# Performance work log

Hardware: AMD Instinct MI355X
Metric: run time of the kernel (lower is better)

Reference implementation:

```python
import jax, jax.numpy as jnp
import numpy as np
import math

B, L, D, H = 2, 2048, 1024, 16
DT = D // H  # d_tensor per head


def setup_inputs() -> dict:
    key = jax.random.key(0)
    ks = jax.random.split(key, 14)
    s = 1.0 / math.sqrt(D)
    return {
        "Q": jax.random.normal(ks[0], (B, L, D), jnp.float32),
        "K": jax.random.normal(ks[1], (B, L, D), jnp.float32),
        "V": jax.random.normal(ks[2], (B, L, D), jnp.float32),
        "mask": jax.random.randint(ks[3], (B, L, L), 0, 2, jnp.int32),
        "attn_bias": jax.random.normal(ks[4], (1, H, L, L), jnp.float32),
        "Wq": jax.random.normal(ks[5], (D, D), jnp.float32) * s,
        "bq": jnp.zeros((D,), jnp.float32),
        "Wk": jax.random.normal(ks[6], (D, D), jnp.float32) * s,
        "bk": jnp.zeros((D,), jnp.float32),
        "Wv": jax.random.normal(ks[7], (D, D), jnp.float32) * s,
        "bv": jnp.zeros((D,), jnp.float32),
        "Wo": jax.random.normal(ks[8], (D, D), jnp.float32) * s,
        "bo": jnp.zeros((D,), jnp.float32),
    }


def _split(x):
    # (B, L, D) -> (B, H, L, DT)
    b, l, d = x.shape
    return x.reshape(b, l, H, DT).transpose(0, 2, 1, 3)


def reference(Q, K, V, mask, attn_bias, Wq, bq, Wk, bk, Wv, bv, Wo, bo):
    # Linear projections (torch nn.Linear: x @ W.T + b)
    q = _split(Q @ Wq.T + bq)  # (B, H, L, DT)
    k = _split(K @ Wk.T + bk)
    v = _split(V @ Wv.T + bv)
    scale = 1.0 / math.sqrt(DT)
    score = jnp.einsum("bhqd,bhkd->bhqk", q, k) * scale  # (B, H, L, L)
    # masked_fill(mask==0, -10000), mask broadcast over heads
    score = jnp.where(mask[:, None, :, :] == 0, jnp.float32(-10000.0), score)
    # encoder path: additive attn_bias (is_dec_layer=False)
    score = score + attn_bias
    p = jax.nn.softmax(score, axis=-1)
    out = jnp.einsum("bhqk,bhkd->bhqd", p, v)  # (B, H, L, DT)
    out = out.transpose(0, 2, 1, 3).reshape(Q.shape[0], Q.shape[1], D)
    return out @ Wo.T + bo
```

## Files before the change

kernel.cpp:

```cpp
#include <hip/hip_runtime.h>
#include <hip/hip_bf16.h>

#define NB 2
#define NL 2048
#define ND 1024
#define NH 16
#define NDT 64
#define SZE ((size_t)NB * NL * ND)
#define WSZE ((size_t)ND * ND)

typedef unsigned short u16;
typedef unsigned int u32;
typedef unsigned long long u64;

typedef __attribute__((ext_vector_type(8))) short s16x8;
typedef __attribute__((ext_vector_type(4))) float f32x4;
typedef __attribute__((ext_vector_type(4))) u16 u16x4;
typedef __attribute__((ext_vector_type(8))) u16 u16x8;

static __device__ __forceinline__ u16 f2b(float f) {
  union { float f; u32 u; } x; x.f = f;
  u32 r = x.u + 0x7fffu + ((x.u >> 16) & 1u);
  return (u16)(r >> 16);
}

static __device__ __forceinline__ int swz(int r, int cb) {
  return r * 128 + (cb ^ ((r & 7) << 4));
}

static __device__ __forceinline__ void gl16(const void* g, void* l) {
  __builtin_amdgcn_global_load_lds(
      (const __attribute__((address_space(1))) unsigned int*)g,
      (__attribute__((address_space(3))) unsigned int*)l, 16, 0, 0);
}

static __device__ __forceinline__ u16x8 pack8(f32x4 a, f32x4 b) {
  u16x8 r;
  r[0] = f2b(a[0]); r[1] = f2b(a[1]); r[2] = f2b(a[2]); r[3] = f2b(a[3]);
  r[4] = f2b(b[0]); r[5] = f2b(b[1]); r[6] = f2b(b[2]); r[7] = f2b(b[3]);
  return r;
}

static __device__ __forceinline__ u64 ldg_v2(const u64* p) {
  u64 r;
  asm volatile("global_load_dwordx2 %0, %1, off" : "=v"(r) : "v"(p) : "memory");
  return r;
}

__global__ __launch_bounds__(256)
void conv_k(const float* __restrict__ q, const float* __restrict__ k,
            const float* __restrict__ v, const float* __restrict__ wq,
            const float* __restrict__ wk, const float* __restrict__ wv,
            const float* __restrict__ wo, u16* __restrict__ cin,
            u16* __restrict__ cw)
{
  const int z = blockIdx.z;
  const float* s; u16* d; size_t n;
  if (z < 3) { s = (z == 0) ? q : (z == 1) ? k : v; d = cin + (size_t)z * SZE; n = SZE; }
  else { int m = z - 3; s = (m == 0) ? wq : (m == 1) ? wk : (m == 2) ? wv : wo; d = cw + (size_t)m * WSZE; n = WSZE; }
  size_t i = ((size_t)blockIdx.x * 256 + threadIdx.x) * 8;
  if (i >= n) return;
  f32x4 a = *reinterpret_cast<const f32x4*>(s + i);
  f32x4 b = *reinterpret_cast<const f32x4*>(s + i + 4);
  *reinterpret_cast<u16x8*>(d + i) = pack8(a, b);
}

__global__ __launch_bounds__(256)
void maskpack_k(const int* __restrict__ mask, u64* __restrict__ mb) {
  const int lane = threadIdx.x & 63;
  const int gw = (blockIdx.x * 256 + threadIdx.x) >> 6;
  const int nw = (gridDim.x * 256) >> 6;
  const int NCH = NB * NL * NL / 64;
  for (int c = gw; c < NCH; c += nw) {
    int v = mask[(size_t)c * 64 + lane];
    u64 bal = __ballot(v != 0);
    if (lane == 0) mb[c] = bal;
  }
}

template<int FINAL>
__global__ __launch_bounds__(256, 2)
void gemm_k(const u16* __restrict__ Abase, const u16* __restrict__ Wbase,
            const float* __restrict__ b0, const float* __restrict__ b1,
            const float* __restrict__ b2, void* __restrict__ outp)
{
  __shared__ __align__(16) u16 lA[2][128 * 64];
  __shared__ __align__(16) u16 lB[2][128 * 64];
  const int tid = threadIdx.x, lane = tid & 63, w = tid >> 6;
  const int wr = w >> 1, wc = w & 1, lrow = lane & 15, lgrp = lane >> 4;
  const int z = FINAL ? 0 : blockIdx.z;
  const u16* A = Abase + (FINAL ? (size_t)0 : (size_t)z * SZE);
  const u16* W = Wbase + (FINAL ? 3 * WSZE : (size_t)z * WSZE);
  const float* bias = FINAL ? b0 : (z == 0 ? b0 : (z == 1) ? b1 : b2);
  const int mbase = blockIdx.y * 128, nbase = blockIdx.x * 128;

  f32x4 acc[4][4] = {};

#define GSTAGE(BUF, T) do {                                                   \
  const int k0 = (T) * 64;                                                    \
  _Pragma("unroll") for (int i = 0; i < 4; ++i) {                             \
    int r = i * 32 + w * 8 + (lane >> 3);                                     \
    int cb = ((lane & 7) << 4) ^ ((r & 7) << 4);                              \
    gl16((const char*)(A + (size_t)(mbase + r) * ND + k0) + cb,               \
         (char*)lA[BUF] + i * 4096 + w * 1024);                               \
    gl16((const char*)(W + (size_t)(nbase + r) * ND + k0) + cb,               \
         (char*)lB[BUF] + i * 4096 + w * 1024);                               \
  }                                                                           \
} while (0)

#define GCOMP(BUF) do {                                                       \
  _Pragma("unroll") for (int ks = 0; ks < 2; ++ks) {                          \
    s16x8 af[4], bf[4];                                                       \
    _Pragma("unroll") for (int t = 0; t < 4; ++t) {                           \
      af[t] = *reinterpret_cast<const s16x8*>((char*)lA[BUF] + swz(wr * 64 + t * 16 + lrow, ks * 64 + lgrp * 16)); \
      bf[t] = *reinterpret_cast<const s16x8*>((char*)lB[BUF] + swz(wc * 64 + t * 16 + lrow, ks * 64 + lgrp * 16)); \
    }                                                                         \
    _Pragma("unroll") for (int mt = 0; mt < 4; ++mt)                          \
      _Pragma("unroll") for (int nt = 0; nt < 4; ++nt)                        \
        acc[mt][nt] = __builtin_amdgcn_mfma_f32_16x16x32_bf16(af[mt], bf[nt], acc[mt][nt], 0, 0, 0); \
  }                                                                           \
} while (0)

  GSTAGE(0, 0);
  __syncthreads();
  int cur = 0;
#pragma unroll 1
  for (int t = 0; t < 15; ++t) {
    GSTAGE(cur ^ 1, t + 1);
    GCOMP(cur);
    __syncthreads();
    cur ^= 1;
  }
  GCOMP(cur);

#pragma unroll
  for (int mt = 0; mt < 4; ++mt) {
#pragma unroll
    for (int nt = 0; nt < 4; ++nt) {
      int n = nbase + wc * 64 + nt * 16 + lrow;
      float bv = bias[n];
      int m0 = mbase + wr * 64 + mt * 16 + lgrp * 4;
      f32x4 a = acc[mt][nt];
      if constexpr (FINAL) {
#pragma unroll
        for (int rg = 0; rg < 4; ++rg)
          ((float*)outp)[(size_t)(m0 + rg) * ND + n] = a[rg] + bv;
      } else {
        int h = n >> 6, d = n & 63;
        if (z == 2) {
          int b = m0 >> 11, l0 = m0 & 2047;
          u16x4 ov;
#pragma unroll
          for (int rg = 0; rg < 4; ++rg) ov[rg] = f2b(a[rg] + bv);
          *reinterpret_cast<u16x4*>((u16*)outp + 2 * SZE + ((size_t)(b * NH + h) * NDT + d) * NL + l0) = ov;
        } else {
#pragma unroll
          for (int rg = 0; rg < 4; ++rg) {
            int m = m0 + rg;
            int b = m >> 11, l = m & 2047;
            ((u16*)outp)[(size_t)z * SZE + ((size_t)(b * NH + h) * NL + l) * NDT + d] = f2b(a[rg] + bv);
          }
        }
      }
    }
  }
#undef GSTAGE
#undef GCOMP
}

__global__ __launch_bounds__(256, 2)
void attn_k(const u16* __restrict__ q, const u16* __restrict__ k,
            const u16* __restrict__ vt, const u64* __restrict__ mb,
            const float* __restrict__ bias, u16* __restrict__ ao)
{
  __shared__ __align__(16) u16 kl2[2][64 * 64];
  __shared__ __align__(16) u16 vl2[2][64 * 64];
  __shared__ __align__(16) float bl2[2][64 * 64];
  __shared__ __align__(16) u16 pl[4][16 * 64];

  const int tid = threadIdx.x;
  const int lane = tid & 63, w = tid >> 6;
  const int lrow = lane & 15, lgrp = lane >> 4;
  const int bid = blockIdx.x;
  const int b = bid & 1;
  const int h = (bid >> 1) & (NH - 1);
  const int qt = bid >> 5;
  const int bh = b * NH + h;
  const int qbase = qt * 64;
  const int qrow = qbase + w * 16 + lrow;
  const int rr = w * 16 + lrow;

  s16x8 qf[2];
#pragma unroll
  for (int ks = 0; ks < 2; ++ks)
    qf[ks] = *reinterpret_cast<const s16x8*>(q + ((size_t)bh * NL + qrow) * NDT + ks * 32 + lgrp * 8);

  f32x4 o4[4] = {};
  float mrun = -3.0e38f, lrun = 0.f;

  const u64* mrow = mb + ((size_t)b * NL + qrow) * (NL / 64);
  u16* pw = pl[w];
  u64 mA, mB;

#define STAGEA(KK, KD, VD, BD) do {                                           \
  const char* ksrc = (const char*)(k + ((size_t)bh * NL + (KK)) * NDT);       \
  _Pragma("unroll") for (int i = 0; i < 2; ++i) {                             \
    int o = i * 4096 + w * 1024 + lane * 16;                                  \
    int r = o >> 7; int cb = (o & 127) ^ ((r & 7) << 4);                      \
    gl16(ksrc + r * 128 + cb, (char*)(KD) + i * 4096 + w * 1024);             \
    gl16((const char*)vt + (((size_t)bh * NDT + r) * NL + (KK)) * 2 + cb,     \
         (char*)(VD) + i * 4096 + w * 1024);                                  \
  }                                                                           \
  _Pragma("unroll") for (int i = 0; i < 4; ++i) {                             \
    int r = i * 16 + w * 4 + lgrp;                                            \
    int c = lane & 15;                                                        \
    gl16((const char*)(bias + ((size_t)h * NL + qbase + r) * NL + (KK)) +     \
             ((c ^ (r & 15)) << 4),                                           \
         (char*)(BD) + i * 4096 + w * 1024);                                  \
  }                                                                           \
} while (0)

#define TILE(KD, VD, BD, MM) do {                                             \
  float sv[4][4];                                                             \
  _Pragma("unroll") for (int nt = 0; nt < 4; ++nt) {                          \
    f32x4 s = {};                                                             \
    _Pragma("unroll") for (int ks = 0; ks < 2; ++ks) {                        \
      s16x8 kf = *reinterpret_cast<const s16x8*>((char*)(KD) + swz(nt * 16 + lrow, ks * 64 + lgrp * 16)); \
      s = __builtin_amdgcn_mfma_f32_16x16x32_bf16(kf, qf[ks], s, 0, 0, 0);    \
    }                                                                         \
    f32x4 bf = *reinterpret_cast<const f32x4*>((const char*)(BD) + rr * 256 + ((((nt << 2) + lgrp) ^ lrow) << 4)); \
    _Pragma("unroll") for (int rg = 0; rg < 4; ++rg) {                        \
      int sh = nt * 16 + lgrp * 4 + rg;                                       \
      sv[nt][rg] = ((MM >> sh) & 1ull) ? s[rg] * 0.125f + bf[rg] : bf[rg] - 10000.0f; \
    }                                                                         \
  }                                                                           \
  float mx = sv[0][0];                                                        \
  _Pragma("unroll") for (int nt = 0; nt < 4; ++nt)                            \
    _Pragma("unroll") for (int rg = 0; rg < 4; ++rg) mx = fmaxf(mx, sv[nt][rg]); \
  mx = fmaxf(mx, __shfl_xor(mx, 16)); mx = fmaxf(mx, __shfl_xor(mx, 32));     \
  float mnew = fmaxf(mrun, mx);                                               \
  float alpha = __expf(mrun - mnew); mrun = mnew;                             \
  float rs = 0.f;                                                             \
  _Pragma("unroll") for (int nt = 0; nt < 4; ++nt)                            \
    _Pragma("unroll") for (int rg = 0; rg < 4; ++rg) {                        \
      float p = __expf(sv[nt][rg] - mnew); sv[nt][rg] = p; rs += p;           \
    }                                                                         \
  rs += __shfl_xor(rs, 16); rs += __shfl_xor(rs, 32);                         \
  lrun = lrun * alpha + rs;                                                   \
  _Pragma("unroll") for (int dt = 0; dt < 4; ++dt)                            \
    _Pragma("unroll") for (int rg = 0; rg < 4; ++rg) o4[dt][rg] *= alpha;     \
  _Pragma("unroll") for (int nt = 0; nt < 4; ++nt) {                          \
    u16x4 pk;                                                                 \
    _Pragma("unroll") for (int rg = 0; rg < 4; ++rg) pk[rg] = f2b(sv[nt][rg]); \
    *reinterpret_cast<u16x4*>((char*)pw + swz(lrow, nt * 32 + lgrp * 8)) = pk; \
  }                                                                           \
  s16x8 pa0 = *reinterpret_cast<const s16x8*>((char*)pw + swz(lrow, lgrp * 16)); \
  s16x8 pa1 = *reinterpret_cast<const s16x8*>((char*)pw + swz(lrow, 64 + lgrp * 16)); \
  _Pragma("unroll") for (int dt = 0; dt < 4; ++dt) {                          \
    s16x8 vf0 = *reinterpret_cast<const s16x8*>((char*)(VD) + swz(dt * 16 + lrow, lgrp * 16)); \
    o4[dt] = __builtin_amdgcn_mfma_f32_16x16x32_bf16(vf0, pa0, o4[dt], 0, 0, 0); \
    s16x8 vf1 = *reinterpret_cast<const s16x8*>((char*)(VD) + swz(dt * 16 + lrow, 64 + lgrp * 16)); \
    o4[dt] = __builtin_amdgcn_mfma_f32_16x16x32_bf16(vf1, pa1, o4[dt], 0, 0, 0); \
  }                                                                           \
} while (0)

  STAGEA(0, kl2[0], vl2[0], bl2[0]);
  mA = ldg_v2(mrow + 0);
  __syncthreads();

#pragma unroll 1
  for (int tt = 0; tt < NL / 64; tt += 2) {
    STAGEA((tt + 1) * 64, kl2[1], vl2[1], bl2[1]);
    mB = ldg_v2(mrow + tt + 1);
    TILE(kl2[0], vl2[0], bl2[0], mA);
    __syncthreads();
    if (tt + 2 < NL / 64) {
      STAGEA((tt + 2) * 64, kl2[0], vl2[0], bl2[0]);
      mA = ldg_v2(mrow + tt + 2);
    }
    TILE(kl2[1], vl2[1], bl2[1], mB);
    __syncthreads();
  }

  float inv = 1.0f / lrun;
#pragma unroll
  for (int dt = 0; dt < 4; ++dt) {
    u16x4 ov;
#pragma unroll
    for (int rg = 0; rg < 4; ++rg) ov[rg] = f2b(o4[dt][rg] * inv);
    *reinterpret_cast<u16x4*>(ao + ((size_t)(b * NL + qrow)) * ND + h * NDT + dt * 16 + lgrp * 4) = ov;
  }
#undef STAGEA
#undef TILE
}

extern "C" void kernel_launch(void* const* d_in, const int* in_sizes, int n_in,
                              void* d_out, int out_size, void* d_ws, size_t ws_size,
                              hipStream_t stream)
{
  const float* Q    = (const float*)d_in[0];
  const float* K    = (const float*)d_in[1];
  const float* V    = (const float*)d_in[2];
  const int*   mask = (const int*)d_in[3];
  const float* bias = (const float*)d_in[4];
  const float* Wq   = (const float*)d_in[5];
  const float* bq   = (const float*)d_in[6];
  const float* Wk   = (const float*)d_in[7];
  const float* bk   = (const float*)d_in[8];
  const float* Wv   = (const float*)d_in[9];
  const float* bv   = (const float*)d_in[10];
  const float* Wo   = (const float*)d_in[11];
  const float* bo   = (const float*)d_in[12];

  u16* cin  = (u16*)d_ws;
  u16* cw   = cin + 3 * SZE;
  u16* qkv  = cw + 4 * WSZE;
  u64* mbit = (u64*)(qkv + 3 * SZE);
  u16* aob  = cin;

  dim3 blk(256);

  conv_k<<<dim3(2048, 1, 7), blk, 0, stream>>>(Q, K, V, Wq, Wk, Wv, Wo, cin, cw);
  maskpack_k<<<dim3(1024), blk, 0, stream>>>(mask, mbit);

  gemm_k<0><<<dim3(ND / 128, (NB * NL) / 128, 3), blk, 0, stream>>>(cin, cw, bq, bk, bv, qkv);

  attn_k<<<dim3(NB * NH * (NL / 64)), blk, 0, stream>>>(qkv, qkv + SZE, qkv + 2 * SZE, mbit, bias, aob);

  gemm_k<1><<<dim3(ND / 128, (NB * NL) / 128), blk, 0, stream>>>(aob, cw, bo, bo, bo, d_out);
}
```

Before: 245.8 us.

## Load attention bias directly into registers and use exp2 with lazy rescaling

The attention bias tile is no longer staged through shared memory. Each lane now loads its bias values straight into registers with global vector loads, prefetched one tile ahead, which cuts LDS usage and LDS traffic. Softmax moves to base-2 exponentials with the scale folded into one FMA, and the running-max rescale of the accumulator is skipped when the new max stays within a threshold. It also adds s_setprio around the MFMA sections, switches to the library bf16 conversion, and drops the occupancy hint from the launch bounds. The risks are higher register pressure from the prefetched bias registers and possible exponent growth from the lazy rescaling.

Result: slower. 268.8 us (+9.4%).

```diff
diff --git a/kernel.cpp b/kernel.cpp
--- a/kernel.cpp
+++ b/kernel.cpp
@@ -23,6 +23,10 @@
   u32 r = x.u + 0x7fffu + ((x.u >> 16) & 1u);
   return (u16)(r >> 16);
 }
+static __device__ __forceinline__ u16 f2b16(float f) {
+  __hip_bfloat16 h = __float2bfloat16(f);
+  return *reinterpret_cast<u16*>(&h);
+}
 
 static __device__ __forceinline__ int swz(int r, int cb) {
   return r * 128 + (cb ^ ((r & 7) << 4));
@@ -41,6 +45,11 @@
   return r;
 }
 
+static __device__ __forceinline__ f32x4 ldg_v4(const float* p) {
+  f32x4 r;
+  asm volatile("global_load_dwordx4 %0, %1, off" : "=v"(r) : "v"(p) : "memory");
+  return r;
+}
 static __device__ __forceinline__ u64 ldg_v2(const u64* p) {
   u64 r;
   asm volatile("global_load_dwordx2 %0, %1, off" : "=v"(r) : "v"(p) : "memory");
@@ -168,14 +177,13 @@
 #undef GCOMP
 }
 
-__global__ __launch_bounds__(256, 2)
+__global__ __launch_bounds__(256)
 void attn_k(const u16* __restrict__ q, const u16* __restrict__ k,
             const u16* __restrict__ vt, const u64* __restrict__ mb,
             const float* __restrict__ bias, u16* __restrict__ ao)
 {
   __shared__ __align__(16) u16 kl2[2][64 * 64];
   __shared__ __align__(16) u16 vl2[2][64 * 64];
-  __shared__ __align__(16) float bl2[2][64 * 64];
   __shared__ __align__(16) u16 pl[4][16 * 64];
 
   const int tid = threadIdx.x;
@@ -188,7 +196,10 @@
   const int bh = b * NH + h;
   const int qbase = qt * 64;
   const int qrow = qbase + w * 16 + lrow;
-  const int rr = w * 16 + lrow;
+
+  const float L2E = 1.4426950408889634f;
+  const float SC2 = 0.125f * L2E;
+  const float NEGM = -10000.0f * L2E;
 
   s16x8 qf[2];
 #pragma unroll
@@ -199,10 +210,19 @@
   float mrun = -3.0e38f, lrun = 0.f;
 
   const u64* mrow = mb + ((size_t)b * NL + qrow) * (NL / 64);
+  const float* brow = bias + ((size_t)h * NL + qrow) * NL;
   u16* pw = pl[w];
+
+  f32x4 bA[4], bB[4];
   u64 mA, mB;
 
-#define STAGEA(KK, KD, VD, BD) do {                                           \
+#define LOADPF(BP, MM, KK) do {                                               \
+  _Pragma("unroll") for (int nt = 0; nt < 4; ++nt)                            \
+    BP[nt] = ldg_v4(brow + (KK) + nt * 16 + lgrp * 4);                        \
+  MM = ldg_v2(mrow + ((KK) >> 6));                                            \
+} while (0)
+
+#define STAGEKV(KK, KD, VD) do {                                              \
   const char* ksrc = (const char*)(k + ((size_t)bh * NL + (KK)) * NDT);       \
   _Pragma("unroll") for (int i = 0; i < 2; ++i) {                             \
     int o = i * 4096 + w * 1024 + lane * 16;                                  \
@@ -211,74 +231,75 @@
     gl16((const char*)vt + (((size_t)bh * NDT + r) * NL + (KK)) * 2 + cb,     \
          (char*)(VD) + i * 4096 + w * 1024);                                  \
   }                                                                           \
-  _Pragma("unroll") for (int i = 0; i < 4; ++i) {                             \
-    int r = i * 16 + w * 4 + lgrp;                                            \
-    int c = lane & 15;                                                        \
-    gl16((const char*)(bias + ((size_t)h * NL + qbase + r) * NL + (KK)) +     \
-             ((c ^ (r & 15)) << 4),                                           \
-         (char*)(BD) + i * 4096 + w * 1024);                                  \
-  }                                                                           \
-} while (0)
-
-#define TILE(KD, VD, BD, MM) do {                                             \
+} while (0)
+
+#define TILE(KD, VD, BP, MM) do {                                             \
   float sv[4][4];                                                             \
+  __builtin_amdgcn_s_setprio(1);                                              \
   _Pragma("unroll") for (int nt = 0; nt < 4; ++nt) {                          \
     f32x4 s = {};                                                             \
     _Pragma("unroll") for (int ks = 0; ks < 2; ++ks) {                        \
       s16x8 kf = *reinterpret_cast<const s16x8*>((char*)(KD) + swz(nt * 16 + lrow, ks * 64 + lgrp * 16)); \
       s = __builtin_amdgcn_mfma_f32_16x16x32_bf16(kf, qf[ks], s, 0, 0, 0);    \
     }                                                                         \
-    f32x4 bf = *reinterpret_cast<const f32x4*>((const char*)(BD) + rr * 256 + ((((nt << 2) + lgrp) ^ lrow) << 4)); \
     _Pragma("unroll") for (int rg = 0; rg < 4; ++rg) {                        \
       int sh = nt * 16 + lgrp * 4 + rg;                                       \
-      sv[nt][rg] = ((MM >> sh) & 1ull) ? s[rg] * 0.125f + bf[rg] : bf[rg] - 10000.0f; \
+      float t = BP[nt][rg] * L2E;                                             \
+      sv[nt][rg] = ((MM >> sh) & 1ull) ? __builtin_fmaf(s[rg], SC2, t) : t + NEGM; \
     }                                                                         \
   }                                                                           \
+  __builtin_amdgcn_s_setprio(0);                                              \
   float mx = sv[0][0];                                                        \
   _Pragma("unroll") for (int nt = 0; nt < 4; ++nt)                            \
     _Pragma("unroll") for (int rg = 0; rg < 4; ++rg) mx = fmaxf(mx, sv[nt][rg]); \
   mx = fmaxf(mx, __shfl_xor(mx, 16)); mx = fmaxf(mx, __shfl_xor(mx, 32));     \
-  float mnew = fmaxf(mrun, mx);                                               \
-  float alpha = __expf(mrun - mnew); mrun = mnew;                             \
+  if (!__all(mx <= mrun + 8.0f)) {                                            \
+    float mnew = fmaxf(mrun, mx);                                             \
+    float alpha = exp2f(mrun - mnew);                                         \
+    mrun = mnew;                                                              \
+    lrun *= alpha;                                                            \
+    _Pragma("unroll") for (int dt = 0; dt < 4; ++dt)                          \
+      _Pragma("unroll") for (int rg = 0; rg < 4; ++rg) o4[dt][rg] *= alpha;   \
+  }                                                                           \
   float rs = 0.f;                                                             \
   _Pragma("unroll") for (int nt = 0; nt < 4; ++nt)                            \
     _Pragma("unroll") for (int rg = 0; rg < 4; ++rg) {                        \
-      float p = __expf(sv[nt][rg] - mnew); sv[nt][rg] = p; rs += p;           \
+      float p = exp2f(sv[nt][rg] - mrun); sv[nt][rg] = p; rs += p;            \
     }                                                                         \
   rs += __shfl_xor(rs, 16); rs += __shfl_xor(rs, 32);                         \
-  lrun = lrun * alpha + rs;                                                   \
-  _Pragma("unroll") for (int dt = 0; dt < 4; ++dt)                            \
-    _Pragma("unroll") for (int rg = 0; rg < 4; ++rg) o4[dt][rg] *= alpha;     \
+  lrun += rs;                                                                 \
   _Pragma("unroll") for (int nt = 0; nt < 4; ++nt) {                          \
     u16x4 pk;                                                                 \
-    _Pragma("unroll") for (int rg = 0; rg < 4; ++rg) pk[rg] = f2b(sv[nt][rg]); \
+    _Pragma("unroll") for (int rg = 0; rg < 4; ++rg) pk[rg] = f2b16(sv[nt][rg]); \
     *reinterpret_cast<u16x4*>((char*)pw + swz(lrow, nt * 32 + lgrp * 8)) = pk; \
   }                                                                           \
   s16x8 pa0 = *reinterpret_cast<const s16x8*>((char*)pw + swz(lrow, lgrp * 16)); \
   s16x8 pa1 = *reinterpret_cast<const s16x8*>((char*)pw + swz(lrow, 64 + lgrp * 16)); \
+  __builtin_amdgcn_s_setprio(1);                                              \
   _Pragma("unroll") for (int dt = 0; dt < 4; ++dt) {                          \
     s16x8 vf0 = *reinterpret_cast<const s16x8*>((char*)(VD) + swz(dt * 16 + lrow, lgrp * 16)); \
     o4[dt] = __builtin_amdgcn_mfma_f32_16x16x32_bf16(vf0, pa0, o4[dt], 0, 0, 0); \
     s16x8 vf1 = *reinterpret_cast<const s16x8*>((char*)(VD) + swz(dt * 16 + lrow, 64 + lgrp * 16)); \
     o4[dt] = __builtin_amdgcn_mfma_f32_16x16x32_bf16(vf1, pa1, o4[dt], 0, 0, 0); \
   }                                                                           \
-} while (0)
-
-  STAGEA(0, kl2[0], vl2[0], bl2[0]);
-  mA = ldg_v2(mrow + 0);
+  __builtin_amdgcn_s_setprio(0);                                              \
+} while (0)
+
+  STAGEKV(0, kl2[0], vl2[0]);
+  LOADPF(bA, mA, 0);
   __syncthreads();
 
 #pragma unroll 1
   for (int tt = 0; tt < NL / 64; tt += 2) {
-    STAGEA((tt + 1) * 64, kl2[1], vl2[1], bl2[1]);
-    mB = ldg_v2(mrow + tt + 1);
-    TILE(kl2[0], vl2[0], bl2[0], mA);
+    STAGEKV((tt + 1) * 64, kl2[1], vl2[1]);
+    LOADPF(bB, mB, (tt + 1) * 64);
+    TILE(kl2[0], vl2[0], bA, mA);
     __syncthreads();
     if (tt + 2 < NL / 64) {
-      STAGEA((tt + 2) * 64, kl2[0], vl2[0], bl2[0]);
-      mA = ldg_v2(mrow + tt + 2);
+      STAGEKV((tt + 2) * 64, kl2[0], vl2[0]);
+      LOADPF(bA, mA, (tt + 2) * 64);
     }
-    TILE(kl2[1], vl2[1], bl2[1], mB);
+    TILE(kl2[1], vl2[1], bB, mB);
     __syncthreads();
   }
 
@@ -287,10 +308,11 @@
   for (int dt = 0; dt < 4; ++dt) {
     u16x4 ov;
 #pragma unroll
-    for (int rg = 0; rg < 4; ++rg) ov[rg] = f2b(o4[dt][rg] * inv);
+    for (int rg = 0; rg < 4; ++rg) ov[rg] = f2b16(o4[dt][rg] * inv);
     *reinterpret_cast<u16x4*>(ao + ((size_t)(b * NL + qrow)) * ND + h * NDT + dt * 16 + lgrp * 4) = ov;
   }
-#undef STAGEA
+#undef LOADPF
+#undef STAGEKV
 #undef TILE
 }
 
```

## Pipeline GEMM with explicit vmcnt waits and read V directly from global

Applied to the files above, without the earlier changes.

The projection GEMM loop is unrolled by two with fixed buffers, and __syncthreads is replaced by explicit s_waitcnt vmcnt plus s_barrier and sched_barrier fences, so the prefetch of the next tile can stay in flight while the current one is consumed. In the attention kernel, V tiles are no longer staged through LDS. Each lane loads its V fragments straight from global memory inside the PV loop, which frees LDS. The attention kernel's launch_bounds minimum of 2 blocks is dropped. The direct V loads bring global latency into the inner loop and rely on cache hits, and the changed launch bounds may alter register allocation and occupancy.

Measured after the change: 300.9 us. 22.4% more time.

```diff
diff --git a/kernel.cpp b/kernel.cpp
--- a/kernel.cpp
+++ b/kernel.cpp
@@ -17,6 +17,10 @@
 typedef __attribute__((ext_vector_type(4))) float f32x4;
 typedef __attribute__((ext_vector_type(4))) u16 u16x4;
 typedef __attribute__((ext_vector_type(8))) u16 u16x8;
+
+#define VW(N) asm volatile("s_waitcnt vmcnt(" #N ")" ::: "memory")
+#define SB __builtin_amdgcn_s_barrier()
+#define SCB __builtin_amdgcn_sched_barrier(0)
 
 static __device__ __forceinline__ u16 f2b(float f) {
   union { float f; u32 u; } x; x.f = f;
@@ -122,16 +126,23 @@
 } while (0)
 
   GSTAGE(0, 0);
-  __syncthreads();
-  int cur = 0;
 #pragma unroll 1
-  for (int t = 0; t < 15; ++t) {
-    GSTAGE(cur ^ 1, t + 1);
-    GCOMP(cur);
-    __syncthreads();
-    cur ^= 1;
-  }
-  GCOMP(cur);
+  for (int t = 0; t < 14; t += 2) {
+    GSTAGE(1, t + 1);
+    SCB; VW(8); SB; SCB;
+    GCOMP(0);
+    SCB; SB; SCB;
+    GSTAGE(0, t + 2);
+    SCB; VW(8); SB; SCB;
+    GCOMP(1);
+    SCB; SB; SCB;
+  }
+  GSTAGE(1, 15);
+  SCB; VW(8); SB; SCB;
+  GCOMP(0);
+  SCB; SB; SCB;
+  SCB; VW(0); SB; SCB;
+  GCOMP(1);
 
 #pragma unroll
   for (int mt = 0; mt < 4; ++mt) {
@@ -168,13 +179,12 @@
 #undef GCOMP
 }
 
-__global__ __launch_bounds__(256, 2)
+__global__ __launch_bounds__(256)
 void attn_k(const u16* __restrict__ q, const u16* __restrict__ k,
             const u16* __restrict__ vt, const u64* __restrict__ mb,
             const float* __restrict__ bias, u16* __restrict__ ao)
 {
   __shared__ __align__(16) u16 kl2[2][64 * 64];
-  __shared__ __align__(16) u16 vl2[2][64 * 64];
   __shared__ __align__(16) float bl2[2][64 * 64];
   __shared__ __align__(16) u16 pl[4][16 * 64];
 
@@ -199,17 +209,16 @@
   float mrun = -3.0e38f, lrun = 0.f;
 
   const u64* mrow = mb + ((size_t)b * NL + qrow) * (NL / 64);
+  const u16* vlane = vt + (size_t)bh * NDT * NL + (size_t)lrow * NL + lgrp * 8;
   u16* pw = pl[w];
   u64 mA, mB;
 
-#define STAGEA(KK, KD, VD, BD) do {                                           \
+#define STAGEA(KK, KD, BD) do {                                               \
   const char* ksrc = (const char*)(k + ((size_t)bh * NL + (KK)) * NDT);       \
   _Pragma("unroll") for (int i = 0; i < 2; ++i) {                             \
     int o = i * 4096 + w * 1024 + lane * 16;                                  \
     int r = o >> 7; int cb = (o & 127) ^ ((r & 7) << 4);                      \
     gl16(ksrc + r * 128 + cb, (char*)(KD) + i * 4096 + w * 1024);             \
-    gl16((const char*)vt + (((size_t)bh * NDT + r) * NL + (KK)) * 2 + cb,     \
-         (char*)(VD) + i * 4096 + w * 1024);                                  \
   }                                                                           \
   _Pragma("unroll") for (int i = 0; i < 4; ++i) {                             \
     int r = i * 16 + w * 4 + lgrp;                                            \
@@ -220,7 +229,7 @@
   }                                                                           \
 } while (0)
 
-#define TILE(KD, VD, BD, MM) do {                                             \
+#define TILE(KK, KD, BD, MM) do {                                             \
   float sv[4][4];                                                             \
   _Pragma("unroll") for (int nt = 0; nt < 4; ++nt) {                          \
     f32x4 s = {};                                                             \
@@ -257,28 +266,29 @@
   s16x8 pa0 = *reinterpret_cast<const s16x8*>((char*)pw + swz(lrow, lgrp * 16)); \
   s16x8 pa1 = *reinterpret_cast<const s16x8*>((char*)pw + swz(lrow, 64 + lgrp * 16)); \
   _Pragma("unroll") for (int dt = 0; dt < 4; ++dt) {                          \
-    s16x8 vf0 = *reinterpret_cast<const s16x8*>((char*)(VD) + swz(dt * 16 + lrow, lgrp * 16)); \
+    const u16* vrow = vlane + (size_t)(dt * 16) * NL + (KK);                  \
+    s16x8 vf0 = *reinterpret_cast<const s16x8*>(vrow);                        \
     o4[dt] = __builtin_amdgcn_mfma_f32_16x16x32_bf16(vf0, pa0, o4[dt], 0, 0, 0); \
-    s16x8 vf1 = *reinterpret_cast<const s16x8*>((char*)(VD) + swz(dt * 16 + lrow, 64 + lgrp * 16)); \
+    s16x8 vf1 = *reinterpret_cast<const s16x8*>(vrow + 32);                   \
     o4[dt] = __builtin_amdgcn_mfma_f32_16x16x32_bf16(vf1, pa1, o4[dt], 0, 0, 0); \
   }                                                                           \
 } while (0)
 
-  STAGEA(0, kl2[0], vl2[0], bl2[0]);
+  STAGEA(0, kl2[0], bl2[0]);
   mA = ldg_v2(mrow + 0);
   __syncthreads();
 
 #pragma unroll 1
   for (int tt = 0; tt < NL / 64; tt += 2) {
-    STAGEA((tt + 1) * 64, kl2[1], vl2[1], bl2[1]);
+    STAGEA((tt + 1) * 64, kl2[1], bl2[1]);
     mB = ldg_v2(mrow + tt + 1);
-    TILE(kl2[0], vl2[0], bl2[0], mA);
+    TILE(tt * 64, kl2[0], bl2[0], mA);
     __syncthreads();
     if (tt + 2 < NL / 64) {
-      STAGEA((tt + 2) * 64, kl2[0], vl2[0], bl2[0]);
+      STAGEA((tt + 2) * 64, kl2[0], bl2[0]);
       mA = ldg_v2(mrow + tt + 2);
     }
-    TILE(kl2[1], vl2[1], bl2[1], mB);
+    TILE((tt + 1) * 64, kl2[1], bl2[1], mB);
     __syncthreads();
   }
 
```

## Replace syncthreads with partial vmcnt waits to keep next tile loads in flight

Applied to the files above, without the earlier changes.

The GEMM and attention main loops now use explicit s_waitcnt vmcnt(N) plus raw s_barrier instead of __syncthreads. Each wait drains only the previous stage's global-to-LDS loads, so the prefetch of the next tile stays outstanding during compute. The GEMM loop is unrolled by two with fixed buffer indices. The attention kernel's launch_bounds drops the min-blocks-per-SM hint, which allows more registers at the possible cost of occupancy. Correctness depends on the hard-coded vmcnt counts matching the number of loads issued per stage.

Result: no change. 249.9 us (+1.7%).

```diff
diff --git a/kernel.cpp b/kernel.cpp
--- a/kernel.cpp
+++ b/kernel.cpp
@@ -17,6 +17,9 @@
 typedef __attribute__((ext_vector_type(4))) float f32x4;
 typedef __attribute__((ext_vector_type(4))) u16 u16x4;
 typedef __attribute__((ext_vector_type(8))) u16 u16x8;
+
+#define VW(N) asm volatile("s_waitcnt vmcnt(" #N ")" ::: "memory")
+#define SB __builtin_amdgcn_s_barrier()
 
 static __device__ __forceinline__ u16 f2b(float f) {
   union { float f; u32 u; } x; x.f = f;
@@ -122,16 +125,23 @@
 } while (0)
 
   GSTAGE(0, 0);
-  __syncthreads();
-  int cur = 0;
 #pragma unroll 1
-  for (int t = 0; t < 15; ++t) {
-    GSTAGE(cur ^ 1, t + 1);
-    GCOMP(cur);
-    __syncthreads();
-    cur ^= 1;
-  }
-  GCOMP(cur);
+  for (int t = 0; t < 14; t += 2) {
+    GSTAGE(1, t + 1);
+    VW(8); SB;
+    GCOMP(0);
+    SB;
+    GSTAGE(0, t + 2);
+    VW(8); SB;
+    GCOMP(1);
+    SB;
+  }
+  GSTAGE(1, 15);
+  VW(8); SB;
+  GCOMP(0);
+  SB;
+  VW(0); SB;
+  GCOMP(1);
 
 #pragma unroll
   for (int mt = 0; mt < 4; ++mt) {
@@ -168,7 +178,7 @@
 #undef GCOMP
 }
 
-__global__ __launch_bounds__(256, 2)
+__global__ __launch_bounds__(256)
 void attn_k(const u16* __restrict__ q, const u16* __restrict__ k,
             const u16* __restrict__ vt, const u64* __restrict__ mb,
             const float* __restrict__ bias, u16* __restrict__ ao)
@@ -266,20 +276,24 @@
 
   STAGEA(0, kl2[0], vl2[0], bl2[0]);
   mA = ldg_v2(mrow + 0);
-  __syncthreads();
 
 #pragma unroll 1
   for (int tt = 0; tt < NL / 64; tt += 2) {
     STAGEA((tt + 1) * 64, kl2[1], vl2[1], bl2[1]);
     mB = ldg_v2(mrow + tt + 1);
+    VW(9); SB;
     TILE(kl2[0], vl2[0], bl2[0], mA);
-    __syncthreads();
+    SB;
     if (tt + 2 < NL / 64) {
       STAGEA((tt + 2) * 64, kl2[0], vl2[0], bl2[0]);
       mA = ldg_v2(mrow + tt + 2);
+      VW(9);
+    } else {
+      VW(0);
     }
+    SB;
     TILE(kl2[1], vl2[1], bl2[1], mB);
-    __syncthreads();
+    SB;
   }
 
   float inv = 1.0f / lrun;
```
